# Optimization experiments

Measured on AMD Instinct MI355X. Metric: run time of the kernel, lower is better.

## Reference

```python
import jax, jax.numpy as jnp
import numpy as np

N, E, G, D, H, C = 50000, 800000, 64, 128, 4, 32
EPS = 1e-5  # GraphNorm eps


def _gcn(x, W, b, src, dst, n):
    # PyG GCNConv: add self-loops (done by caller), symmetric norm D^-1/2 A D^-1/2
    xw = x @ W
    deg = jax.ops.segment_sum(jnp.ones_like(dst, dtype=xw.dtype), dst, num_segments=n)
    dinv = jnp.where(deg > 0, jax.lax.rsqrt(jnp.maximum(deg, 1e-12)), 0.0)
    norm = dinv[src] * dinv[dst]                      # [E2]
    out = jax.ops.segment_sum(xw[src] * norm[:, None], dst, num_segments=n)
    return out + b


def _gat(x, W, a_src, a_dst, b, src, dst, n):
    # PyG GATConv, heads=H, out C per head, concat, leaky_relu slope 0.2, self-loops added by caller
    h = (x @ W).reshape(n, H, C)
    es = jnp.einsum('nhc,hc->nh', h, a_src)
    ed = jnp.einsum('nhc,hc->nh', h, a_dst)
    e = jax.nn.leaky_relu(es[src] + ed[dst], 0.2)     # [E2,H]
    m = jax.ops.segment_max(e, dst, num_segments=n)   # per-dst softmax (stable)
    e = jnp.exp(e - m[dst])
    s = jax.ops.segment_sum(e, dst, num_segments=n)
    alpha = e / (s[dst] + 1e-16)
    out = jax.ops.segment_sum(h[src] * alpha[:, :, None], dst, num_segments=n)
    return out.reshape(n, H * C) + b


def _graphnorm(x, batch, w, b, ms, g):
    cnt = jnp.maximum(jax.ops.segment_sum(jnp.ones((x.shape[0],), x.dtype), batch, num_segments=g), 1.0)
    mean = jax.ops.segment_sum(x, batch, num_segments=g) / cnt[:, None]
    sub = x - ms * mean[batch]
    var = jax.ops.segment_sum(sub * sub, batch, num_segments=g) / cnt[:, None]
    return w * sub * jax.lax.rsqrt(var[batch] + EPS) + b


def setup_inputs() -> dict:
    key = jax.random.key(0)
    ks = jax.random.split(key, 40)

    def lin(k, din, dout):
        return jax.random.normal(k, (din, dout), jnp.float32) * np.float32((2.0 / (din + dout)) ** 0.5)

    inp = {
        'x': jax.random.normal(ks[0], (N, D), jnp.float32),
        'edge_index': jax.random.randint(ks[1], (2, E), 0, N, dtype=jnp.int32),
        'batch': jnp.sort(jax.random.randint(ks[2], (N,), 0, G, dtype=jnp.int32)),
        'Wp': lin(ks[3], D, D), 'bp': jnp.zeros((D,), jnp.float32),
        'Wg': lin(ks[4], D, D), 'bg': jnp.zeros((D,), jnp.float32),
        'Wa1': lin(ks[5], D, H * C), 'as1': jax.random.normal(ks[6], (H, C), jnp.float32) * 0.1,
        'ad1': jax.random.normal(ks[7], (H, C), jnp.float32) * 0.1, 'ba1': jnp.zeros((D,), jnp.float32),
        'Wa2': lin(ks[8], D, H * C), 'as2': jax.random.normal(ks[9], (H, C), jnp.float32) * 0.1,
        'ad2': jax.random.normal(ks[10], (H, C), jnp.float32) * 0.1, 'ba2': jnp.zeros((D,), jnp.float32),
        'gnw0': jnp.ones((D,), jnp.float32), 'gnb0': jnp.zeros((D,), jnp.float32), 'gns0': jnp.ones((D,), jnp.float32),
        'gnw1': jnp.ones((D,), jnp.float32), 'gnb1': jnp.zeros((D,), jnp.float32), 'gns1': jnp.ones((D,), jnp.float32),
        'gnw2': jnp.ones((D,), jnp.float32), 'gnb2': jnp.zeros((D,), jnp.float32), 'gns2': jnp.ones((D,), jnp.float32),
        'hw1': lin(ks[11], 2 * D, D), 'hb1': jnp.zeros((D,), jnp.float32),
        'hw2': lin(ks[12], D, D // 2), 'hb2': jnp.zeros((D // 2,), jnp.float32),
        'hw3': lin(ks[13], D // 2, 2), 'hb3': jnp.zeros((2,), jnp.float32),
        'nw1': lin(ks[14], D, D // 2), 'nb1': jnp.zeros((D // 2,), jnp.float32),
        'nw2': lin(ks[15], D // 2, 1), 'nb2': jnp.zeros((1,), jnp.float32),
    }
    return inp


def reference(x, edge_index, batch, Wp, bp, Wg, bg, Wa1, as1, ad1, ba1, Wa2, as2, ad2, ba2,
              gnw0, gnb0, gns0, gnw1, gnb1, gns1, gnw2, gnb2, gns2,
              hw1, hb1, hw2, hb2, hw3, hb3, nw1, nb1, nw2, nb2):
    n = x.shape[0]
    loop = jnp.arange(n, dtype=edge_index.dtype)
    src = jnp.concatenate([edge_index[0], loop])
    dst = jnp.concatenate([edge_index[1], loop])

    x = x @ Wp + bp
    h = _graphnorm(_gcn(x, Wg, bg, src, dst, n), batch, gnw0, gnb0, gns0, G)
    x = jax.nn.relu(h) + x  # dropout is identity in eval mode
    h = _graphnorm(_gat(x, Wa1, as1, ad1, ba1, src, dst, n), batch, gnw1, gnb1, gns1, G)
    x = jax.nn.relu(h) + x
    h = _graphnorm(_gat(x, Wa2, as2, ad2, ba2, src, dst, n), batch, gnw2, gnb2, gns2, G)
    x = jax.nn.relu(h) + x

    node_hub_scores = jax.nn.sigmoid((jax.nn.relu(x @ nw1 + nb1) @ nw2 + nb2)[:, 0])

    cnt = jnp.maximum(jax.ops.segment_sum(jnp.ones((n,), x.dtype), batch, num_segments=G), 1.0)
    gmean = jax.ops.segment_sum(x, batch, num_segments=G) / cnt[:, None]
    gmax = jax.ops.segment_max(x, batch, num_segments=G)
    graph_features = jnp.concatenate([gmean, gmax], axis=1)  # [G, 2D]

    z = jax.nn.relu(graph_features @ hw1 + hb1)
    z = jax.nn.relu(z @ hw2 + hb2)
    logits = z @ hw3 + hb3
    return (logits, node_hub_scores, graph_features, x)
```

## Files before the change

### kernel.cpp

```cpp
#include <hip/hip_runtime.h>
#include <cstdint>

#define D 128
#define GG 64
#define SLICES 16
#define NXCD 8

typedef short bf16x8 __attribute__((ext_vector_type(8)));
typedef float f32x4 __attribute__((ext_vector_type(4)));

__device__ inline unsigned short bf16u(float f) {
  unsigned u = __float_as_uint(f);
  u = (u + 0x7FFFu + ((u >> 16) & 1u)) >> 16;
  return (unsigned short)u;
}
__device__ inline float2 unpackbf2(unsigned u) {
  return make_float2(__uint_as_float(u << 16), __uint_as_float(u & 0xFFFF0000u));
}
__device__ inline void accum8(float* acc, uint4 v, float w) {
  float2 p0 = unpackbf2(v.x), p1 = unpackbf2(v.y), p2 = unpackbf2(v.z), p3 = unpackbf2(v.w);
  acc[0] += p0.x * w; acc[1] += p0.y * w; acc[2] += p1.x * w; acc[3] += p1.y * w;
  acc[4] += p2.x * w; acc[5] += p2.y * w; acc[6] += p3.x * w; acc[7] += p3.y * w;
}

__global__ void count_edges_k(const int* __restrict__ dst, int* __restrict__ cnt, int E) {
  int e = blockIdx.x * blockDim.x + threadIdx.x;
  if (e < E) atomicAdd(&cnt[dst[e]], 1);
}

__global__ void bounds_init_k(int* __restrict__ gstart, int* __restrict__ gend) {
  int g = threadIdx.x;
  gstart[g] = 0;
  gend[g] = 0;
}

__global__ void graph_bounds_k(const int* __restrict__ batch, int* __restrict__ gstart,
                               int* __restrict__ gend, int n) {
  int i = blockIdx.x * blockDim.x + threadIdx.x;
  if (i >= n) return;
  int b = batch[i];
  if (i == 0) {
    gstart[b] = 0;
  } else {
    int pb = batch[i - 1];
    if (pb != b) { gstart[b] = i; gend[pb] = i; }
  }
  if (i == n - 1) gend[b] = n;
}

__global__ void gcnt_k(const int* __restrict__ gstart, const int* __restrict__ gend,
                       int* __restrict__ gcnt) {
  int g = threadIdx.x;
  gcnt[g] = gend[g] - gstart[g];
}

__global__ __launch_bounds__(256) void scan1_k(const int* __restrict__ cnt, int* __restrict__ rp,
                                               int* __restrict__ bsum, int n) {
  __shared__ int sd[256];
  int t = threadIdx.x;
  int i = blockIdx.x * 256 + t;
  int v = (i < n) ? cnt[i] : 0;
  sd[t] = v;
  __syncthreads();
#pragma unroll
  for (int off = 1; off < 256; off <<= 1) {
    int u = (t >= off) ? sd[t - off] : 0;
    __syncthreads();
    sd[t] += u;
    __syncthreads();
  }
  if (i < n) rp[i] = sd[t] - v;
  if (t == 255) bsum[blockIdx.x] = sd[255];
}

__global__ __launch_bounds__(256) void scan2_k(int* __restrict__ bsum, int nb) {
  __shared__ int sd[256];
  int t = threadIdx.x;
  int v = (t < nb) ? bsum[t] : 0;
  sd[t] = v;
  __syncthreads();
#pragma unroll
  for (int off = 1; off < 256; off <<= 1) {
    int u = (t >= off) ? sd[t - off] : 0;
    __syncthreads();
    sd[t] += u;
    __syncthreads();
  }
  if (t < nb) bsum[t] = sd[t] - v;
}

__global__ __launch_bounds__(256) void scan3_k(int* __restrict__ rp, const int* __restrict__ bsum,
                                               int* __restrict__ cur, const int* __restrict__ cnt,
                                               float* __restrict__ dinv, int n, int E) {
  int i = blockIdx.x * 256 + threadIdx.x;
  if (i < n) {
    int r = rp[i] + bsum[blockIdx.x];
    rp[i] = r;
    cur[i] = r;
    dinv[i] = rsqrtf((float)cnt[i] + 1.0f);
  }
  if (i == 0) rp[n] = E;
}

__global__ __launch_bounds__(256) void fill_csr_xcd_k(const int* __restrict__ src,
                                                      const int* __restrict__ dst,
                                                      int* __restrict__ cur,
                                                      unsigned short* __restrict__ col,
                                                      int E, int slice) {
  int pass = blockIdx.x & (NXCD - 1);
  int e = (blockIdx.x >> 3) * 256 + threadIdx.x;
  if (e >= E) return;
  int d = dst[e];
  if ((unsigned)(d - pass * slice) < (unsigned)slice) {
    int p = atomicAdd(&cur[d], 1);
    col[p] = (unsigned short)src[e];
  }
}

__global__ void cast_bf16_k(const float* __restrict__ in, unsigned short* __restrict__ outp, int n4) {
  int i = blockIdx.x * blockDim.x + threadIdx.x;
  if (i >= n4) return;
  float4 v = ((const float4*)in)[i];
  ushort4 o;
  o.x = bf16u(v.x); o.y = bf16u(v.y); o.z = bf16u(v.z); o.w = bf16u(v.w);
  ((ushort4*)outp)[i] = o;
}

__global__ void packB_k(const float* __restrict__ B, unsigned short* __restrict__ Bp, int ldb, int ct) {
  int idx = blockIdx.x * 256 + threadIdx.x;
  if (idx >= ct * 256) return;
  int lane = idx & 63;
  int kc = (idx >> 6) & 3;
  int c = idx >> 8;
  int kb = kc * 32 + (lane >> 4) * 8;
  int colq = c * 16 + (lane & 15);
  unsigned short o[8];
#pragma unroll
  for (int j = 0; j < 8; ++j) o[j] = bf16u(B[(size_t)(kb + j) * ldb + colq]);
  uint4 p;
  p.x = (unsigned)o[0] | ((unsigned)o[1] << 16);
  p.y = (unsigned)o[2] | ((unsigned)o[3] << 16);
  p.z = (unsigned)o[4] | ((unsigned)o[5] << 16);
  p.w = (unsigned)o[6] | ((unsigned)o[7] << 16);
  *(uint4*)&Bp[(size_t)idx * 8] = p;
}

__global__ __launch_bounds__(256) void gemm_mfma_k(const unsigned short* __restrict__ Ab,
                                                   const unsigned short* __restrict__ Bp,
                                                   const float* __restrict__ bias,
                                                   float* __restrict__ Cf,
                                                   unsigned short* __restrict__ Cb, int M) {
  __shared__ unsigned short Bs[16384];
  int t = threadIdx.x;
  for (int i = t; i < 2048; i += 256) ((uint4*)Bs)[i] = ((const uint4*)Bp)[i];
  __syncthreads();
  int w = t >> 6, lane = t & 63;
  int row0 = blockIdx.x * 64 + w * 16;
  int arow = row0 + (lane & 15);
  f32x4 acc[8];
#pragma unroll
  for (int c = 0; c < 8; ++c) acc[c] = {0.f, 0.f, 0.f, 0.f};
#pragma unroll
  for (int kc = 0; kc < 4; ++kc) {
    bf16x8 a = {0, 0, 0, 0, 0, 0, 0, 0};
    if (arow < M) a = *(const bf16x8*)&Ab[(size_t)arow * 128 + kc * 32 + (lane >> 4) * 8];
#pragma unroll
    for (int c = 0; c < 8; ++c) {
      bf16x8 b = *(const bf16x8*)&Bs[((c * 4 + kc) * 64 + lane) * 8];
      acc[c] = __builtin_amdgcn_mfma_f32_16x16x32_bf16(a, b, acc[c], 0, 0, 0);
    }
  }
  int rbase = row0 + (lane >> 4) * 4;
#pragma unroll
  for (int c = 0; c < 8; ++c) {
    int colq = c * 16 + (lane & 15);
    float bb = bias ? bias[colq] : 0.f;
#pragma unroll
    for (int r = 0; r < 4; ++r) {
      int row = rbase + r;
      if (row < M) {
        float v = acc[c][r] + bb;
        if (Cf) Cf[(size_t)row * 128 + colq] = v;
        if (Cb) Cb[(size_t)row * 128 + colq] = bf16u(v);
      }
    }
  }
}

__global__ __launch_bounds__(256) void gcn_gather_k(const uint4* __restrict__ xw16,
                                                    const int* __restrict__ rp,
                                                    const unsigned short* __restrict__ col,
                                                    const float* __restrict__ dinv, const float* __restrict__ bias,
                                                    float* __restrict__ out, int n) {
  int i = blockIdx.x * 4 + (threadIdx.x >> 6);
  if (i >= n) return;
  int lane = threadIdx.x & 63;
  int g = lane >> 4, sub = lane & 15;
  int e0 = __builtin_amdgcn_readfirstlane(rp[i]);
  int e1 = __builtin_amdgcn_readfirstlane(rp[i + 1]);
  float di = dinv[i];
  float acc[8] = {0.f, 0.f, 0.f, 0.f, 0.f, 0.f, 0.f, 0.f};
  if (g == 0) {
    uint4 v = xw16[(size_t)i * 16 + sub];
    accum8(acc, v, di * di);
  }
  int e = e0;
  for (; e + 15 < e1; e += 16) {
    int s0 = col[e + g];
    int s1 = col[e + 4 + g];
    int s2 = col[e + 8 + g];
    int s3 = col[e + 12 + g];
    float w0 = dinv[s0] * di, w1 = dinv[s1] * di, w2 = dinv[s2] * di, w3 = dinv[s3] * di;
    uint4 v0 = xw16[(size_t)s0 * 16 + sub];
    uint4 v1 = xw16[(size_t)s1 * 16 + sub];
    uint4 v2 = xw16[(size_t)s2 * 16 + sub];
    uint4 v3 = xw16[(size_t)s3 * 16 + sub];
    accum8(acc, v0, w0); accum8(acc, v1, w1); accum8(acc, v2, w2); accum8(acc, v3, w3);
  }
  for (; e < e1; e += 4) {
    bool ok = (e + g) < e1;
    int s0 = ok ? (int)col[e + g] : i;
    float w0 = ok ? dinv[s0] * di : 0.f;
    uint4 v0 = xw16[(size_t)s0 * 16 + sub];
    accum8(acc, v0, w0);
  }
#pragma unroll
  for (int k = 0; k < 8; ++k) {
    acc[k] += __shfl_xor(acc[k], 16, 64);
    acc[k] += __shfl_xor(acc[k], 32, 64);
  }
  if (g == 0) {
    float4 b0 = ((const float4*)bias)[sub * 2], b1 = ((const float4*)bias)[sub * 2 + 1];
    *(float4*)&out[(size_t)i * 128 + sub * 8] =
        make_float4(acc[0] + b0.x, acc[1] + b0.y, acc[2] + b0.z, acc[3] + b0.w);
    *(float4*)&out[(size_t)i * 128 + sub * 8 + 4] =
        make_float4(acc[4] + b1.x, acc[5] + b1.y, acc[6] + b1.z, acc[7] + b1.w);
  }
}

__global__ void attn_coef_k(const unsigned short* __restrict__ hb, const float* __restrict__ a_s,
                            const float* __restrict__ a_d, float* __restrict__ es,
                            float* __restrict__ ed, int n) {
  int idx = blockIdx.x * blockDim.x + threadIdx.x;
  if (idx >= n * 4) return;
  int node = idx >> 2, hh = idx & 3;
  const uint4* hr = (const uint4*)(hb + (size_t)node * 128 + hh * 32);
  const float4* av = (const float4*)(a_s + hh * 32);
  const float4* dv = (const float4*)(a_d + hh * 32);
  float s = 0.f, d2 = 0.f;
#pragma unroll
  for (int q = 0; q < 4; ++q) {
    uint4 u = hr[q];
    float2 p0 = unpackbf2(u.x), p1 = unpackbf2(u.y), p2 = unpackbf2(u.z), p3 = unpackbf2(u.w);
    float4 a0 = av[q * 2], a1 = av[q * 2 + 1];
    float4 d0 = dv[q * 2], d1 = dv[q * 2 + 1];
    s  += p0.x * a0.x + p0.y * a0.y + p1.x * a0.z + p1.y * a0.w
        + p2.x * a1.x + p2.y * a1.y + p3.x * a1.z + p3.y * a1.w;
    d2 += p0.x * d0.x + p0.y * d0.y + p1.x * d0.z + p1.y * d0.w
        + p2.x * d1.x + p2.y * d1.y + p3.x * d1.z + p3.y * d1.w;
  }
  es[idx] = s;
  ed[idx] = d2;
}

__global__ __launch_bounds__(256) void alpha_k(const float* __restrict__ es, const float* __restrict__ ed,
                                               const int* __restrict__ rp,
                                               const unsigned short* __restrict__ col,
                                               float* __restrict__ alpha, float* __restrict__ aself,
                                               float* __restrict__ winv, int n) {
  int i = blockIdx.x * 4 + (threadIdx.x >> 6);
  if (i >= n) return;
  int lane = threadIdx.x & 63;
  int hh = lane >> 4, slot = lane & 15;
  int e0 = __builtin_amdgcn_readfirstlane(rp[i]);
  int e1 = __builtin_amdgcn_readfirstlane(rp[i + 1]);
  float edi = ed[i * 4 + hh];
  float esf = es[i * 4 + hh] + edi;
  esf = esf >= 0.f ? esf : 0.2f * esf;
  float m = esf;
  for (int e = e0 + slot; e < e1; e += 16) {
    int sj = col[e];
    float ev = es[sj * 4 + hh] + edi;
    ev = ev >= 0.f ? ev : 0.2f * ev;
    alpha[(size_t)e * 4 + hh] = ev;
    m = fmaxf(m, ev);
  }
#pragma unroll
  for (int off = 1; off < 16; off <<= 1) m = fmaxf(m, __shfl_xor(m, off, 64));
  float s = (slot == 0) ? __expf(esf - m) : 0.f;
  for (int e = e0 + slot; e < e1; e += 16) {
    float w = __expf(alpha[(size_t)e * 4 + hh] - m);
    alpha[(size_t)e * 4 + hh] = w;
    s += w;
  }
#pragma unroll
  for (int off = 1; off < 16; off <<= 1) s += __shfl_xor(s, off, 64);
  if (slot == 0) {
    aself[i * 4 + hh] = __expf(esf - m);
    winv[i * 4 + hh] = 1.0f / (s + 1e-16f);
  }
}

__global__ __launch_bounds__(256) void gat_gather_k(const uint4* __restrict__ hf16,
                                                    const int* __restrict__ rp,
                                                    const unsigned short* __restrict__ col,
                                                    const float* __restrict__ alpha, const float* __restrict__ aself,
                                                    const float* __restrict__ winv,
                                                    const float* __restrict__ bias, float* __restrict__ out, int n) {
  int i = blockIdx.x * 4 + (threadIdx.x >> 6);
  if (i >= n) return;
  int lane = threadIdx.x & 63;
  int g = lane >> 4, sub = lane & 15;
  int hh = sub >> 2;
  int e0 = __builtin_amdgcn_readfirstlane(rp[i]);
  int e1 = __builtin_amdgcn_readfirstlane(rp[i + 1]);
  float acc[8] = {0.f, 0.f, 0.f, 0.f, 0.f, 0.f, 0.f, 0.f};
  if (g == 0) {
    uint4 v = hf16[(size_t)i * 16 + sub];
    accum8(acc, v, aself[i * 4 + hh]);
  }
  int e = e0;
  for (; e + 15 < e1; e += 16) {
    int s0 = col[e + g];
    int s1 = col[e + 4 + g];
    int s2 = col[e + 8 + g];
    int s3 = col[e + 12 + g];
    float a0 = alpha[(size_t)(e + g) * 4 + hh];
    float a1 = alpha[(size_t)(e + 4 + g) * 4 + hh];
    float a2 = alpha[(size_t)(e + 8 + g) * 4 + hh];
    float a3 = alpha[(size_t)(e + 12 + g) * 4 + hh];
    uint4 v0 = hf16[(size_t)s0 * 16 + sub];
    uint4 v1 = hf16[(size_t)s1 * 16 + sub];
    uint4 v2 = hf16[(size_t)s2 * 16 + sub];
    uint4 v3 = hf16[(size_t)s3 * 16 + sub];
    accum8(acc, v0, a0); accum8(acc, v1, a1); accum8(acc, v2, a2); accum8(acc, v3, a3);
  }
  for (; e < e1; e += 4) {
    bool ok = (e + g) < e1;
    int s0 = ok ? (int)col[e + g] : i;
    float a0 = ok ? alpha[(size_t)(e + g) * 4 + hh] : 0.f;
    uint4 v0 = hf16[(size_t)s0 * 16 + sub];
    accum8(acc, v0, a0);
  }
#pragma unroll
  for (int k = 0; k < 8; ++k) {
    acc[k] += __shfl_xor(acc[k], 16, 64);
    acc[k] += __shfl_xor(acc[k], 32, 64);
  }
  if (g == 0) {
    float wi = winv[i * 4 + hh];
    float4 b0 = ((const float4*)bias)[sub * 2], b1 = ((const float4*)bias)[sub * 2 + 1];
    *(float4*)&out[(size_t)i * 128 + sub * 8] =
        make_float4(acc[0] * wi + b0.x, acc[1] * wi + b0.y, acc[2] * wi + b0.z, acc[3] * wi + b0.w);
    *(float4*)&out[(size_t)i * 128 + sub * 8 + 4] =
        make_float4(acc[4] * wi + b1.x, acc[5] * wi + b1.y, acc[6] * wi + b1.z, acc[7] * wi + b1.w);
  }
}

__global__ __launch_bounds__(256) void gn_stats_k(const float* __restrict__ h, const int* __restrict__ gstart,
                                                  const int* __restrict__ gcnt, float* __restrict__ gsum,
                                                  float* __restrict__ gsq) {
  int g = blockIdx.x / SLICES, sl = blockIdx.x % SLICES;
  int st = gstart[g], cn = gcnt[g];
  int d = threadIdx.x & 127, half = threadIdx.x >> 7;
  float s = 0.f, ss = 0.f;
  for (int r = sl * 2 + half; r < cn; r += 2 * SLICES) {
    float v = h[(size_t)(st + r) * D + d];
    s += v; ss += v * v;
  }
  __shared__ float l1[128], l2[128];
  if (half) { l1[d] = s; l2[d] = ss; }
  __syncthreads();
  if (!half) {
    atomicAdd(&gsum[g * D + d], s + l1[d]);
    atomicAdd(&gsq[g * D + d], ss + l2[d]);
  }
}

__global__ void gn_finalize_k(const float* __restrict__ gsum, const float* __restrict__ gsq,
                              const int* __restrict__ gcnt, const float* __restrict__ ms,
                              float* __restrict__ mean, float* __restrict__ rstd) {
  int g = blockIdx.x, d = threadIdx.x;
  float cnt = fmaxf((float)gcnt[g], 1.0f);
  float mu = gsum[g * D + d] / cnt;
  float m2 = gsq[g * D + d] / cnt;
  float s = ms[d];
  float var = m2 - (2.0f * s - s * s) * mu * mu;
  mean[g * D + d] = mu;
  rstd[g * D + d] = rsqrtf(fmaxf(var, 0.0f) + 1e-5f);
}

__global__ void gn_apply_k(const float* __restrict__ h, float* __restrict__ x,
                           unsigned short* __restrict__ xb,
                           const int* __restrict__ batch, const float* __restrict__ mean,
                           const float* __restrict__ rstd, const float* __restrict__ w,
                           const float* __restrict__ b, const float* __restrict__ ms, int n) {
  int idx = blockIdx.x * blockDim.x + threadIdx.x;
  if (idx >= n * 32) return;
  int node = idx >> 5, q = idx & 31;
  int g = batch[node];
  int d0 = q * 4;
  float4 hv = ((const float4*)h)[idx];
  float4 xv = ((const float4*)x)[idx];
  float ha[4] = {hv.x, hv.y, hv.z, hv.w};
  float xa[4] = {xv.x, xv.y, xv.z, xv.w};
  float ra[4];
#pragma unroll
  for (int j = 0; j < 4; ++j) {
    int d = d0 + j;
    float sub = ha[j] - ms[d] * mean[g * D + d];
    float v = w[d] * sub * rstd[g * D + d] + b[d];
    ra[j] = fmaxf(v, 0.f) + xa[j];
  }
  ((float4*)x)[idx] = make_float4(ra[0], ra[1], ra[2], ra[3]);
  ushort4 o;
  o.x = bf16u(ra[0]); o.y = bf16u(ra[1]); o.z = bf16u(ra[2]); o.w = bf16u(ra[3]);
  ((ushort4*)xb)[idx] = o;
}

__global__ __launch_bounds__(256) void hub_mfma_k(const unsigned short* __restrict__ Xb,
                                                  const unsigned short* __restrict__ W1p,
                                                  const float* __restrict__ nb1, const float* __restrict__ nw2,
                                                  const float* __restrict__ nb2, float* __restrict__ out, int n) {
  __shared__ unsigned short Bs[8192];
  int t = threadIdx.x;
  for (int i = t; i < 1024; i += 256) ((uint4*)Bs)[i] = ((const uint4*)W1p)[i];
  __syncthreads();
  int w = t >> 6, lane = t & 63;
  int row0 = blockIdx.x * 64 + w * 16;
  int arow = row0 + (lane & 15);
  f32x4 acc[4];
#pragma unroll
  for (int c = 0; c < 4; ++c) acc[c] = {0.f, 0.f, 0.f, 0.f};
#pragma unroll
  for (int kc = 0; kc < 4; ++kc) {
    bf16x8 a = {0, 0, 0, 0, 0, 0, 0, 0};
    if (arow < n) a = *(const bf16x8*)&Xb[(size_t)arow * 128 + kc * 32 + (lane >> 4) * 8];
#pragma unroll
    for (int c = 0; c < 4; ++c) {
      bf16x8 b = *(const bf16x8*)&Bs[((c * 4 + kc) * 64 + lane) * 8];
      acc[c] = __builtin_amdgcn_mfma_f32_16x16x32_bf16(a, b, acc[c], 0, 0, 0);
    }
  }
  float b2 = nb2[0];
  float s[4] = {0.f, 0.f, 0.f, 0.f};
#pragma unroll
  for (int c = 0; c < 4; ++c) {
    int colq = c * 16 + (lane & 15);
    float b1 = nb1[colq];
    float w2 = nw2[colq];
#pragma unroll
    for (int r = 0; r < 4; ++r) s[r] += fmaxf(acc[c][r] + b1, 0.f) * w2;
  }
#pragma unroll
  for (int off = 1; off < 16; off <<= 1) {
#pragma unroll
    for (int r = 0; r < 4; ++r) s[r] += __shfl_xor(s[r], off, 64);
  }
  if ((lane & 15) == 0) {
    int rbase = row0 + (lane >> 4) * 4;
#pragma unroll
    for (int r = 0; r < 4; ++r) {
      int row = rbase + r;
      if (row < n) out[row] = 1.0f / (1.0f + __expf(-(s[r] + b2)));
    }
  }
}

__global__ void init_maxu_k(unsigned* __restrict__ p, int n) {
  int i = blockIdx.x * blockDim.x + threadIdx.x;
  if (i < n) p[i] = 0x007FFFFFu;
}

__global__ __launch_bounds__(256) void pool_stats_k(const float* __restrict__ x, const int* __restrict__ gstart,
                                                    const int* __restrict__ gcnt, float* __restrict__ gsum,
                                                    unsigned* __restrict__ gmaxu) {
  int g = blockIdx.x / SLICES, sl = blockIdx.x % SLICES;
  int st = gstart[g], cn = gcnt[g];
  int d = threadIdx.x & 127, half = threadIdx.x >> 7;
  float s = 0.f, mx = __uint_as_float(0xFF800000u);
  for (int r = sl * 2 + half; r < cn; r += 2 * SLICES) {
    float v = x[(size_t)(st + r) * D + d];
    s += v; mx = fmaxf(mx, v);
  }
  __shared__ float l1[128], l2[128];
  if (half) { l1[d] = s; l2[d] = mx; }
  __syncthreads();
  if (!half) {
    s += l1[d];
    mx = fmaxf(mx, l2[d]);
    atomicAdd(&gsum[g * D + d], s);
    unsigned u = __float_as_uint(mx);
    u = (u & 0x80000000u) ? ~u : (u | 0x80000000u);
    atomicMax(&gmaxu[g * D + d], u);
  }
}

__global__ void pool_fin_k(const float* __restrict__ gsum, const unsigned* __restrict__ gmaxu,
                           const int* __restrict__ gcnt, float* __restrict__ gf) {
  int g = blockIdx.x, d = threadIdx.x;
  float cnt = fmaxf((float)gcnt[g], 1.0f);
  gf[g * 256 + d] = gsum[g * D + d] / cnt;
  unsigned u = gmaxu[g * D + d];
  unsigned bits = (u & 0x80000000u) ? (u ^ 0x80000000u) : ~u;
  gf[g * 256 + 128 + d] = __uint_as_float(bits);
}

__global__ __launch_bounds__(128) void mlp_k(const float* __restrict__ gf, const float* __restrict__ hw1,
                                             const float* __restrict__ hb1, const float* __restrict__ hw2,
                                             const float* __restrict__ hb2, const float* __restrict__ hw3,
                                             const float* __restrict__ hb3, float* __restrict__ logits) {
  __shared__ float sg[256], z1[128], z2[64];
  int g = blockIdx.x, t = threadIdx.x;
  sg[t] = gf[g * 256 + t];
  sg[t + 128] = gf[g * 256 + 128 + t];
  __syncthreads();
  float a = hb1[t];
  for (int k = 0; k < 256; ++k) a += sg[k] * hw1[k * 128 + t];
  z1[t] = fmaxf(a, 0.f);
  __syncthreads();
  if (t < 64) {
    float a2 = hb2[t];
    for (int k = 0; k < 128; ++k) a2 += z1[k] * hw2[k * 64 + t];
    z2[t] = fmaxf(a2, 0.f);
  }
  __syncthreads();
  if (t < 2) {
    float a3 = hb3[t];
    for (int k = 0; k < 64; ++k) a3 += z2[k] * hw3[k * 2 + t];
    logits[g * 2 + t] = a3;
  }
}

extern "C" void kernel_launch(void* const* d_in, const int* in_sizes, int n_in,
                              void* d_out, int out_size, void* d_ws, size_t ws_size,
                              hipStream_t stream) {
  const float* x_in  = (const float*)d_in[0];
  const int*   eidx  = (const int*)d_in[1];
  const int*   batch = (const int*)d_in[2];
  const float* Wp  = (const float*)d_in[3];
  const float* bp  = (const float*)d_in[4];
  const float* Wg  = (const float*)d_in[5];
  const float* bg  = (const float*)d_in[6];
  const float* Wa1 = (const float*)d_in[7];
  const float* as1 = (const float*)d_in[8];
  const float* ad1 = (const float*)d_in[9];
  const float* ba1 = (const float*)d_in[10];
  const float* Wa2 = (const float*)d_in[11];
  const float* as2 = (const float*)d_in[12];
  const float* ad2 = (const float*)d_in[13];
  const float* ba2 = (const float*)d_in[14];
  const float* gnw[3] = {(const float*)d_in[15], (const float*)d_in[18], (const float*)d_in[21]};
  const float* gnb[3] = {(const float*)d_in[16], (const float*)d_in[19], (const float*)d_in[22]};
  const float* gns[3] = {(const float*)d_in[17], (const float*)d_in[20], (const float*)d_in[23]};
  const float* hw1 = (const float*)d_in[24];
  const float* hb1 = (const float*)d_in[25];
  const float* hw2 = (const float*)d_in[26];
  const float* hb2 = (const float*)d_in[27];
  const float* hw3 = (const float*)d_in[28];
  const float* hb3 = (const float*)d_in[29];
  const float* nw1 = (const float*)d_in[30];
  const float* nb1 = (const float*)d_in[31];
  const float* nw2 = (const float*)d_in[32];
  const float* nb2 = (const float*)d_in[33];

  const int N = in_sizes[0] / D;
  const int E = in_sizes[1] / 2;
  const int* src = eidx;
  const int* dst = eidx + E;

  float* out    = (float*)d_out;
  float* logits = out;
  float* hub    = out + GG * 2;
  float* gf     = out + GG * 2 + N;
  float* X      = out + GG * 2 + N + GG * 256;

  char* wp = (char*)d_ws;
  auto alloc = [&](size_t bytes) { char* p = wp; wp += (bytes + 255) & ~(size_t)255; return p; };
  float*    B1    = (float*)alloc((size_t)N * D * 4);
  float*    B2    = (float*)alloc((size_t)N * D * 4);
  unsigned* B1h   = (unsigned*)alloc((size_t)N * (D / 2) * 4);
  unsigned short* Xb = (unsigned short*)alloc((size_t)N * D * 2);
  unsigned short* col = (unsigned short*)alloc((size_t)E * 2);
  int*   cnt     = (int*)alloc((size_t)N * 4);
  int*   rowp    = (int*)alloc((size_t)(N + 1) * 4);
  int*   cur     = (int*)alloc((size_t)N * 4);
  float* dinv    = (float*)alloc((size_t)N * 4);
  float* es      = (float*)alloc((size_t)N * 4 * 4);
  float* ed      = (float*)alloc((size_t)N * 4 * 4);
  float* aself   = (float*)alloc((size_t)N * 4 * 4);
  float* winv    = (float*)alloc((size_t)N * 4 * 4);
  float* gsum    = (float*)alloc((size_t)GG * D * 4);
  float* gsq     = (float*)alloc((size_t)GG * D * 4);
  unsigned* gmaxu = (unsigned*)alloc((size_t)GG * D * 4);
  float* mean    = (float*)alloc((size_t)GG * D * 4);
  float* rstd    = (float*)alloc((size_t)GG * D * 4);
  int*   gcnt    = (int*)alloc((size_t)GG * 4);
  int*   gstart  = (int*)alloc((size_t)GG * 4);
  int*   gend    = (int*)alloc((size_t)GG * 4);
  int*   bsum    = (int*)alloc((size_t)256 * 4);
  unsigned short* Wpp  = (unsigned short*)alloc(16384 * 2);
  unsigned short* Wgp  = (unsigned short*)alloc(16384 * 2);
  unsigned short* Wa1p = (unsigned short*)alloc(16384 * 2);
  unsigned short* Wa2p = (unsigned short*)alloc(16384 * 2);
  unsigned short* W1p  = (unsigned short*)alloc(8192 * 2);
  float* alpha = B1;
  unsigned short* xinb = (unsigned short*)B2;
  if ((size_t)(wp - (char*)d_ws) > ws_size) return;

  const int nb = (N + 255) / 256;

  hipMemsetAsync(cnt, 0, (size_t)N * 4, stream);
  count_edges_k<<<(E + 255) / 256, 256, 0, stream>>>(dst, cnt, E);
  bounds_init_k<<<1, GG, 0, stream>>>(gstart, gend);
  graph_bounds_k<<<nb, 256, 0, stream>>>(batch, gstart, gend, N);
  gcnt_k<<<1, GG, 0, stream>>>(gstart, gend, gcnt);
  scan1_k<<<nb, 256, 0, stream>>>(cnt, rowp, bsum, N);
  scan2_k<<<1, 256, 0, stream>>>(bsum, nb);
  scan3_k<<<nb, 256, 0, stream>>>(rowp, bsum, cur, cnt, dinv, N, E);
  {
    int chunks = (E + 255) / 256;
    int slice = (N + NXCD - 1) / NXCD;
    fill_csr_xcd_k<<<chunks * NXCD, 256, 0, stream>>>(src, dst, cur, col, E, slice);
  }

  packB_k<<<8, 256, 0, stream>>>(Wp, Wpp, 128, 8);
  packB_k<<<8, 256, 0, stream>>>(Wg, Wgp, 128, 8);
  packB_k<<<8, 256, 0, stream>>>(Wa1, Wa1p, 128, 8);
  packB_k<<<8, 256, 0, stream>>>(Wa2, Wa2p, 128, 8);
  packB_k<<<4, 256, 0, stream>>>(nw1, W1p, 64, 4);
  cast_bf16_k<<<(N * 32 + 255) / 256, 256, 0, stream>>>(x_in, xinb, N * 32);

  const int gemmGrid = (N + 63) / 64;
  const int aggGrid  = (N + 3) / 4;

  auto graphnorm = [&](int layer) {
    hipMemsetAsync(gsum, 0, 2 * (size_t)GG * D * 4, stream);
    gn_stats_k<<<GG * SLICES, 256, 0, stream>>>(B2, gstart, gcnt, gsum, gsq);
    gn_finalize_k<<<GG, D, 0, stream>>>(gsum, gsq, gcnt, gns[layer], mean, rstd);
    gn_apply_k<<<(N * 32 + 255) / 256, 256, 0, stream>>>(B2, X, Xb, batch, mean, rstd,
                                                         gnw[layer], gnb[layer], gns[layer], N);
  };

  gemm_mfma_k<<<gemmGrid, 256, 0, stream>>>(xinb, Wpp, bp, X, Xb, N);

  gemm_mfma_k<<<gemmGrid, 256, 0, stream>>>(Xb, Wgp, nullptr, nullptr, (unsigned short*)B1h, N);
  gcn_gather_k<<<aggGrid, 256, 0, stream>>>((const uint4*)B1h, rowp, col, dinv, bg, B2, N);
  graphnorm(0);

  gemm_mfma_k<<<gemmGrid, 256, 0, stream>>>(Xb, Wa1p, nullptr, nullptr, (unsigned short*)B1h, N);
  attn_coef_k<<<(N * 4 + 255) / 256, 256, 0, stream>>>((const unsigned short*)B1h, as1, ad1, es, ed, N);
  alpha_k<<<aggGrid, 256, 0, stream>>>(es, ed, rowp, col, alpha, aself, winv, N);
  gat_gather_k<<<aggGrid, 256, 0, stream>>>((const uint4*)B1h, rowp, col, alpha, aself, winv, ba1, B2, N);
  graphnorm(1);

  gemm_mfma_k<<<gemmGrid, 256, 0, stream>>>(Xb, Wa2p, nullptr, nullptr, (unsigned short*)B1h, N);
  attn_coef_k<<<(N * 4 + 255) / 256, 256, 0, stream>>>((const unsigned short*)B1h, as2, ad2, es, ed, N);
  alpha_k<<<aggGrid, 256, 0, stream>>>(es, ed, rowp, col, alpha, aself, winv, N);
  gat_gather_k<<<aggGrid, 256, 0, stream>>>((const uint4*)B1h, rowp, col, alpha, aself, winv, ba2, B2, N);
  graphnorm(2);

  hub_mfma_k<<<gemmGrid, 256, 0, stream>>>(Xb, W1p, nb1, nw2, nb2, hub, N);

  hipMemsetAsync(gsum, 0, (size_t)GG * D * 4, stream);
  init_maxu_k<<<(GG * D + 255) / 256, 256, 0, stream>>>(gmaxu, GG * D);
  pool_stats_k<<<GG * SLICES, 256, 0, stream>>>(X, gstart, gcnt, gsum, gmaxu);
  pool_fin_k<<<GG, D, 0, stream>>>(gsum, gmaxu, gcnt, gf);
  mlp_k<<<GG, 128, 0, stream>>>(gf, hw1, hb1, hw2, hb2, hw3, hb3, logits);
}
```

Baseline: 454.1 us.

## Fuse GAT attention coefficients into GEMM and softmax into gather

```diff
diff --git a/kernel.cpp b/kernel.cpp
--- a/kernel.cpp
+++ b/kernel.cpp
@@ -149,7 +149,12 @@
                                                    const unsigned short* __restrict__ Bp,
                                                    const float* __restrict__ bias,
                                                    float* __restrict__ Cf,
-                                                   unsigned short* __restrict__ Cb, int M) {
+                                                   unsigned short* __restrict__ Cb,
+                                                   const float* __restrict__ rowscale,
+                                                   const float* __restrict__ as_flat,
+                                                   const float* __restrict__ ad_flat,
+                                                   float* __restrict__ es, float* __restrict__ ed,
+                                                   int M) {
   __shared__ unsigned short Bs[16384];
   int t = threadIdx.x;
   for (int i = t; i < 2048; i += 256) ((uint4*)Bs)[i] = ((const uint4*)Bp)[i];
@@ -170,10 +175,11 @@
       acc[c] = __builtin_amdgcn_mfma_f32_16x16x32_bf16(a, b, acc[c], 0, 0, 0);
     }
   }
+  int l15 = lane & 15;
   int rbase = row0 + (lane >> 4) * 4;
 #pragma unroll
   for (int c = 0; c < 8; ++c) {
-    int colq = c * 16 + (lane & 15);
+    int colq = c * 16 + l15;
     float bb = bias ? bias[colq] : 0.f;
 #pragma unroll
     for (int r = 0; r < 4; ++r) {
@@ -181,8 +187,40 @@
       if (row < M) {
         float v = acc[c][r] + bb;
         if (Cf) Cf[(size_t)row * 128 + colq] = v;
-        if (Cb) Cb[(size_t)row * 128 + colq] = bf16u(v);
+        if (Cb) {
+          float rs = rowscale ? rowscale[row] : 1.f;
+          Cb[(size_t)row * 128 + colq] = bf16u(v * rs);
+        }
       }
+    }
+  }
+  if (as_flat) {
+    float pe[4][4], pd[4][4];
+#pragma unroll
+    for (int h = 0; h < 4; ++h) {
+      float a0 = as_flat[h * 32 + l15], a1 = as_flat[h * 32 + 16 + l15];
+      float d0 = ad_flat[h * 32 + l15], d1 = ad_flat[h * 32 + 16 + l15];
+#pragma unroll
+      for (int r = 0; r < 4; ++r) {
+        pe[h][r] = acc[2 * h][r] * a0 + acc[2 * h + 1][r] * a1;
+        pd[h][r] = acc[2 * h][r] * d0 + acc[2 * h + 1][r] * d1;
+      }
+    }
+#pragma unroll
+    for (int off = 1; off < 16; off <<= 1) {
+#pragma unroll
+      for (int h = 0; h < 4; ++h)
+#pragma unroll
+        for (int r = 0; r < 4; ++r) {
+          pe[h][r] += __shfl_xor(pe[h][r], off, 64);
+          pd[h][r] += __shfl_xor(pd[h][r], off, 64);
+        }
+    }
+    int hh = l15 & 3, rr = l15 >> 2;
+    int row = rbase + rr;
+    if (row < M) {
+      es[row * 4 + hh] = pe[hh][rr];
+      ed[row * 4 + hh] = pd[hh][rr];
     }
   }
 }
@@ -198,11 +236,10 @@
   int g = lane >> 4, sub = lane & 15;
   int e0 = __builtin_amdgcn_readfirstlane(rp[i]);
   int e1 = __builtin_amdgcn_readfirstlane(rp[i + 1]);
-  float di = dinv[i];
   float acc[8] = {0.f, 0.f, 0.f, 0.f, 0.f, 0.f, 0.f, 0.f};
   if (g == 0) {
     uint4 v = xw16[(size_t)i * 16 + sub];
-    accum8(acc, v, di * di);
+    accum8(acc, v, 1.f);
   }
   int e = e0;
   for (; e + 15 < e1; e += 16) {
@@ -210,17 +247,16 @@
     int s1 = col[e + 4 + g];
     int s2 = col[e + 8 + g];
     int s3 = col[e + 12 + g];
-    float w0 = dinv[s0] * di, w1 = dinv[s1] * di, w2 = dinv[s2] * di, w3 = dinv[s3] * di;
     uint4 v0 = xw16[(size_t)s0 * 16 + sub];
     uint4 v1 = xw16[(size_t)s1 * 16 + sub];
     uint4 v2 = xw16[(size_t)s2 * 16 + sub];
     uint4 v3 = xw16[(size_t)s3 * 16 + sub];
-    accum8(acc, v0, w0); accum8(acc, v1, w1); accum8(acc, v2, w2); accum8(acc, v3, w3);
+    accum8(acc, v0, 1.f); accum8(acc, v1, 1.f); accum8(acc, v2, 1.f); accum8(acc, v3, 1.f);
   }
   for (; e < e1; e += 4) {
     bool ok = (e + g) < e1;
     int s0 = ok ? (int)col[e + g] : i;
-    float w0 = ok ? dinv[s0] * di : 0.f;
+    float w0 = ok ? 1.f : 0.f;
     uint4 v0 = xw16[(size_t)s0 * 16 + sub];
     accum8(acc, v0, w0);
   }
@@ -230,82 +266,19 @@
     acc[k] += __shfl_xor(acc[k], 32, 64);
   }
   if (g == 0) {
+    float di = dinv[i];
     float4 b0 = ((const float4*)bias)[sub * 2], b1 = ((const float4*)bias)[sub * 2 + 1];
     *(float4*)&out[(size_t)i * 128 + sub * 8] =
-        make_float4(acc[0] + b0.x, acc[1] + b0.y, acc[2] + b0.z, acc[3] + b0.w);
+        make_float4(acc[0] * di + b0.x, acc[1] * di + b0.y, acc[2] * di + b0.z, acc[3] * di + b0.w);
     *(float4*)&out[(size_t)i * 128 + sub * 8 + 4] =
-        make_float4(acc[4] + b1.x, acc[5] + b1.y, acc[6] + b1.z, acc[7] + b1.w);
-  }
-}
-
-__global__ void attn_coef_k(const unsigned short* __restrict__ hb, const float* __restrict__ a_s,
-                            const float* __restrict__ a_d, float* __restrict__ es,
-                            float* __restrict__ ed, int n) {
-  int idx = blockIdx.x * blockDim.x + threadIdx.x;
-  if (idx >= n * 4) return;
-  int node = idx >> 2, hh = idx & 3;
-  const uint4* hr = (const uint4*)(hb + (size_t)node * 128 + hh * 32);
-  const float4* av = (const float4*)(a_s + hh * 32);
-  const float4* dv = (const float4*)(a_d + hh * 32);
-  float s = 0.f, d2 = 0.f;
-#pragma unroll
-  for (int q = 0; q < 4; ++q) {
-    uint4 u = hr[q];
-    float2 p0 = unpackbf2(u.x), p1 = unpackbf2(u.y), p2 = unpackbf2(u.z), p3 = unpackbf2(u.w);
-    float4 a0 = av[q * 2], a1 = av[q * 2 + 1];
-    float4 d0 = dv[q * 2], d1 = dv[q * 2 + 1];
-    s  += p0.x * a0.x + p0.y * a0.y + p1.x * a0.z + p1.y * a0.w
-        + p2.x * a1.x + p2.y * a1.y + p3.x * a1.z + p3.y * a1.w;
-    d2 += p0.x * d0.x + p0.y * d0.y + p1.x * d0.z + p1.y * d0.w
-        + p2.x * d1.x + p2.y * d1.y + p3.x * d1.z + p3.y * d1.w;
-  }
-  es[idx] = s;
-  ed[idx] = d2;
-}
-
-__global__ __launch_bounds__(256) void alpha_k(const float* __restrict__ es, const float* __restrict__ ed,
-                                               const int* __restrict__ rp,
-                                               const unsigned short* __restrict__ col,
-                                               float* __restrict__ alpha, float* __restrict__ aself,
-                                               float* __restrict__ winv, int n) {
-  int i = blockIdx.x * 4 + (threadIdx.x >> 6);
-  if (i >= n) return;
-  int lane = threadIdx.x & 63;
-  int hh = lane >> 4, slot = lane & 15;
-  int e0 = __builtin_amdgcn_readfirstlane(rp[i]);
-  int e1 = __builtin_amdgcn_readfirstlane(rp[i + 1]);
-  float edi = ed[i * 4 + hh];
-  float esf = es[i * 4 + hh] + edi;
-  esf = esf >= 0.f ? esf : 0.2f * esf;
-  float m = esf;
-  for (int e = e0 + slot; e < e1; e += 16) {
-    int sj = col[e];
-    float ev = es[sj * 4 + hh] + edi;
-    ev = ev >= 0.f ? ev : 0.2f * ev;
-    alpha[(size_t)e * 4 + hh] = ev;
-    m = fmaxf(m, ev);
-  }
-#pragma unroll
-  for (int off = 1; off < 16; off <<= 1) m = fmaxf(m, __shfl_xor(m, off, 64));
-  float s = (slot == 0) ? __expf(esf - m) : 0.f;
-  for (int e = e0 + slot; e < e1; e += 16) {
-    float w = __expf(alpha[(size_t)e * 4 + hh] - m);
-    alpha[(size_t)e * 4 + hh] = w;
-    s += w;
-  }
-#pragma unroll
-  for (int off = 1; off < 16; off <<= 1) s += __shfl_xor(s, off, 64);
-  if (slot == 0) {
-    aself[i * 4 + hh] = __expf(esf - m);
-    winv[i * 4 + hh] = 1.0f / (s + 1e-16f);
+        make_float4(acc[4] * di + b1.x, acc[5] * di + b1.y, acc[6] * di + b1.z, acc[7] * di + b1.w);
   }
 }
 
 __global__ __launch_bounds__(256) void gat_gather_k(const uint4* __restrict__ hf16,
                                                     const int* __restrict__ rp,
                                                     const unsigned short* __restrict__ col,
-                                                    const float* __restrict__ alpha, const float* __restrict__ aself,
-                                                    const float* __restrict__ winv,
+                                                    const float* __restrict__ es, const float* __restrict__ ed,
                                                     const float* __restrict__ bias, float* __restrict__ out, int n) {
   int i = blockIdx.x * 4 + (threadIdx.x >> 6);
   if (i >= n) return;
@@ -314,10 +287,16 @@
   int hh = sub >> 2;
   int e0 = __builtin_amdgcn_readfirstlane(rp[i]);
   int e1 = __builtin_amdgcn_readfirstlane(rp[i + 1]);
+  float edi = ed[i * 4 + hh];
   float acc[8] = {0.f, 0.f, 0.f, 0.f, 0.f, 0.f, 0.f, 0.f};
+  float s = 0.f;
   if (g == 0) {
+    float esf = es[i * 4 + hh] + edi;
+    esf = esf >= 0.f ? esf : 0.2f * esf;
+    float wself = __expf(fminf(esf, 80.f));
     uint4 v = hf16[(size_t)i * 16 + sub];
-    accum8(acc, v, aself[i * 4 + hh]);
+    accum8(acc, v, wself);
+    s = wself;
   }
   int e = e0;
   for (; e + 15 < e1; e += 16) {
@@ -325,30 +304,44 @@
     int s1 = col[e + 4 + g];
     int s2 = col[e + 8 + g];
     int s3 = col[e + 12 + g];
-    float a0 = alpha[(size_t)(e + g) * 4 + hh];
-    float a1 = alpha[(size_t)(e + 4 + g) * 4 + hh];
-    float a2 = alpha[(size_t)(e + 8 + g) * 4 + hh];
-    float a3 = alpha[(size_t)(e + 12 + g) * 4 + hh];
+    float t0 = es[s0 * 4 + hh] + edi;
+    float t1 = es[s1 * 4 + hh] + edi;
+    float t2 = es[s2 * 4 + hh] + edi;
+    float t3 = es[s3 * 4 + hh] + edi;
+    t0 = t0 >= 0.f ? t0 : 0.2f * t0;
+    t1 = t1 >= 0.f ? t1 : 0.2f * t1;
+    t2 = t2 >= 0.f ? t2 : 0.2f * t2;
+    t3 = t3 >= 0.f ? t3 : 0.2f * t3;
+    float w0 = __expf(fminf(t0, 80.f));
+    float w1 = __expf(fminf(t1, 80.f));
+    float w2 = __expf(fminf(t2, 80.f));
+    float w3 = __expf(fminf(t3, 80.f));
     uint4 v0 = hf16[(size_t)s0 * 16 + sub];
     uint4 v1 = hf16[(size_t)s1 * 16 + sub];
     uint4 v2 = hf16[(size_t)s2 * 16 + sub];
     uint4 v3 = hf16[(size_t)s3 * 16 + sub];
-    accum8(acc, v0, a0); accum8(acc, v1, a1); accum8(acc, v2, a2); accum8(acc, v3, a3);
+    accum8(acc, v0, w0); accum8(acc, v1, w1); accum8(acc, v2, w2); accum8(acc, v3, w3);
+    s += w0 + w1 + w2 + w3;
   }
   for (; e < e1; e += 4) {
     bool ok = (e + g) < e1;
     int s0 = ok ? (int)col[e + g] : i;
-    float a0 = ok ? alpha[(size_t)(e + g) * 4 + hh] : 0.f;
+    float t0 = es[s0 * 4 + hh] + edi;
+    t0 = t0 >= 0.f ? t0 : 0.2f * t0;
+    float w0 = ok ? __expf(fminf(t0, 80.f)) : 0.f;
     uint4 v0 = hf16[(size_t)s0 * 16 + sub];
-    accum8(acc, v0, a0);
+    accum8(acc, v0, w0);
+    s += w0;
   }
 #pragma unroll
   for (int k = 0; k < 8; ++k) {
     acc[k] += __shfl_xor(acc[k], 16, 64);
     acc[k] += __shfl_xor(acc[k], 32, 64);
   }
+  s += __shfl_xor(s, 16, 64);
+  s += __shfl_xor(s, 32, 64);
   if (g == 0) {
-    float wi = winv[i * 4 + hh];
+    float wi = 1.0f / s;
     float4 b0 = ((const float4*)bias)[sub * 2], b1 = ((const float4*)bias)[sub * 2 + 1];
     *(float4*)&out[(size_t)i * 128 + sub * 8] =
         make_float4(acc[0] * wi + b0.x, acc[1] * wi + b0.y, acc[2] * wi + b0.z, acc[3] * wi + b0.w);
@@ -577,7 +570,6 @@
 
   char* wp = (char*)d_ws;
   auto alloc = [&](size_t bytes) { char* p = wp; wp += (bytes + 255) & ~(size_t)255; return p; };
-  float*    B1    = (float*)alloc((size_t)N * D * 4);
   float*    B2    = (float*)alloc((size_t)N * D * 4);
   unsigned* B1h   = (unsigned*)alloc((size_t)N * (D / 2) * 4);
   unsigned short* Xb = (unsigned short*)alloc((size_t)N * D * 2);
@@ -588,8 +580,6 @@
   float* dinv    = (float*)alloc((size_t)N * 4);
   float* es      = (float*)alloc((size_t)N * 4 * 4);
   float* ed      = (float*)alloc((size_t)N * 4 * 4);
-  float* aself   = (float*)alloc((size_t)N * 4 * 4);
-  float* winv    = (float*)alloc((size_t)N * 4 * 4);
   float* gsum    = (float*)alloc((size_t)GG * D * 4);
   float* gsq     = (float*)alloc((size_t)GG * D * 4);
   unsigned* gmaxu = (unsigned*)alloc((size_t)GG * D * 4);
@@ -604,7 +594,6 @@
   unsigned short* Wa1p = (unsigned short*)alloc(16384 * 2);
   unsigned short* Wa2p = (unsigned short*)alloc(16384 * 2);
   unsigned short* W1p  = (unsigned short*)alloc(8192 * 2);
-  float* alpha = B1;
   unsigned short* xinb = (unsigned short*)B2;
   if ((size_t)(wp - (char*)d_ws) > ws_size) return;
 
@@ -642,22 +631,22 @@
                                                          gnw[layer], gnb[layer], gns[layer], N);
   };
 
-  gemm_mfma_k<<<gemmGrid, 256, 0, stream>>>(xinb, Wpp, bp, X, Xb, N);
-
-  gemm_mfma_k<<<gemmGrid, 256, 0, stream>>>(Xb, Wgp, nullptr, nullptr, (unsigned short*)B1h, N);
+  gemm_mfma_k<<<gemmGrid, 256, 0, stream>>>(xinb, Wpp, bp, X, Xb,
+                                            nullptr, nullptr, nullptr, nullptr, nullptr, N);
+
+  gemm_mfma_k<<<gemmGrid, 256, 0, stream>>>(Xb, Wgp, nullptr, nullptr, (unsigned short*)B1h,
+                                            dinv, nullptr, nullptr, nullptr, nullptr, N);
   gcn_gather_k<<<aggGrid, 256, 0, stream>>>((const uint4*)B1h, rowp, col, dinv, bg, B2, N);
   graphnorm(0);
 
-  gemm_mfma_k<<<gemmGrid, 256, 0, stream>>>(Xb, Wa1p, nullptr, nullptr, (unsigned short*)B1h, N);
-  attn_coef_k<<<(N * 4 + 255) / 256, 256, 0, stream>>>((const unsigned short*)B1h, as1, ad1, es, ed, N);
-  alpha_k<<<aggGrid, 256, 0, stream>>>(es, ed, rowp, col, alpha, aself, winv, N);
-  gat_gather_k<<<aggGrid, 256, 0, stream>>>((const uint4*)B1h, rowp, col, alpha, aself, winv, ba1, B2, N);
+  gemm_mfma_k<<<gemmGrid, 256, 0, stream>>>(Xb, Wa1p, nullptr, nullptr, (unsigned short*)B1h,
+                                            nullptr, as1, ad1, es, ed, N);
+  gat_gather_k<<<aggGrid, 256, 0, stream>>>((const uint4*)B1h, rowp, col, es, ed, ba1, B2, N);
   graphnorm(1);
 
-  gemm_mfma_k<<<gemmGrid, 256, 0, stream>>>(Xb, Wa2p, nullptr, nullptr, (unsigned short*)B1h, N);
-  attn_coef_k<<<(N * 4 + 255) / 256, 256, 0, stream>>>((const unsigned short*)B1h, as2, ad2, es, ed, N);
-  alpha_k<<<aggGrid, 256, 0, stream>>>(es, ed, rowp, col, alpha, aself, winv, N);
-  gat_gather_k<<<aggGrid, 256, 0, stream>>>((const uint4*)B1h, rowp, col, alpha, aself, winv, ba2, B2, N);
+  gemm_mfma_k<<<gemmGrid, 256, 0, stream>>>(Xb, Wa2p, nullptr, nullptr, (unsigned short*)B1h,
+                                            nullptr, as2, ad2, es, ed, N);
+  gat_gather_k<<<aggGrid, 256, 0, stream>>>((const uint4*)B1h, rowp, col, es, ed, ba2, B2, N);
   graphnorm(2);
 
   hub_mfma_k<<<gemmGrid, 256, 0, stream>>>(Xb, W1p, nb1, nw2, nb2, hub, N);
```

New measurement: 414.5 us. 8.7% less time.
